# Kernel optimization log

Measured on AMD Instinct MI355X. Metric: run time of the kernel, lower is better.

## Reference

```python
import jax, jax.numpy as jnp
import numpy as np

INPUT_SIZE = 1024
HIDDEN_SIZE = 1024
BATCH = 8192


def setup_inputs() -> dict:
    key = jax.random.key(0)
    ks = jax.random.split(key, 10)
    H, I, B = HIDDEN_SIZE, INPUT_SIZE, BATCH
    s = 1.0 / np.sqrt(H)  # scale params so activations stay in sane range
    return {
        "input": jax.random.normal(ks[0], (B, I), jnp.float32),
        "hx": jax.random.normal(ks[1], (B, H), jnp.float32),
        "cx": jax.random.normal(ks[2], (B, H), jnp.float32),
        "att": jax.random.normal(ks[3], (B, I), jnp.float32),
        "weight_ih": jax.random.normal(ks[4], (4 * H, I), jnp.float32) * s,
        "weight_hh": jax.random.normal(ks[5], (4 * H, H), jnp.float32) * s,
        "bias_ih": jax.random.normal(ks[6], (4 * H,), jnp.float32),
        "bias_hh": jax.random.normal(ks[7], (4 * H,), jnp.float32),
        "weight_att": jax.random.normal(ks[8], (2 * H, I), jnp.float32) * s,
        "bias_att": jax.random.normal(ks[9], (2 * H,), jnp.float32),
    }


def reference(input, hx, cx, att, weight_ih, weight_hh, bias_ih, bias_hh,
              weight_att, bias_att):
    H = weight_hh.shape[1]
    # gates: [B, 4H]
    gates = input @ weight_ih.T + bias_ih + hx @ weight_hh.T + bias_hh
    att_gates = att @ weight_att.T + bias_att  # [B, 2H]
    ingate, forgetgate, cellgate, outgate = jnp.split(gates, 4, axis=1)
    ingate_att, attgate = jnp.split(att_gates, 2, axis=1)
    ingate = jax.nn.sigmoid(ingate)
    forgetgate = jax.nn.sigmoid(forgetgate)
    cellgate = jnp.tanh(cellgate)
    ingate_att = jax.nn.sigmoid(ingate_att)
    attgate = jnp.tanh(attgate)
    outgate = jax.nn.sigmoid(outgate)
    cy = forgetgate * cx + ingate * cellgate + ingate_att * attgate
    hy = outgate * jnp.tanh(cy)
    return (hy, cy)
```

## Files before the change

kernel.cpp:

```cpp
#include <hip/hip_runtime.h>


typedef __attribute__((ext_vector_type(8))) __bf16 bf16x8;
typedef __attribute__((ext_vector_type(8))) unsigned short ushort8;
typedef __attribute__((ext_vector_type(4))) float f32x4;

#define AS1 __attribute__((address_space(1)))
#define AS3 __attribute__((address_space(3)))

__device__ __forceinline__ void gld16(const unsigned short* g, unsigned short* l) {
    __builtin_amdgcn_global_load_lds((const AS1 void*)g, (AS3 void*)l, 16, 0, 0);
}

__device__ __forceinline__ unsigned short f2bf(float f) {
    unsigned int u = __builtin_bit_cast(unsigned int, f);
    u += 0x7fffu + ((u >> 16) & 1u);
    return (unsigned short)(u >> 16);
}

__device__ __forceinline__ float sigmoidf_(float x) { return 1.f / (1.f + __expf(-x)); }
__device__ __forceinline__ float tanhf_(float x) {
    float e = __expf(-2.f * fabsf(x));
    float t = (1.f - e) / (1.f + e);
    return x >= 0.f ? t : -t;
}

__device__ __forceinline__ bf16x8 ldfrag(const unsigned short* p) {
    return __builtin_bit_cast(bf16x8, *(const ushort8*)p);
}

#define BARRIER __builtin_amdgcn_s_barrier()
#define LGKM0   asm volatile("s_waitcnt lgkmcnt(0)" ::: "memory")
#define VMW_(n) asm volatile("s_waitcnt vmcnt(" #n ")" ::: "memory")
#define VMW(n)  VMW_(n)
#define MFMA16(a, b, c) __builtin_amdgcn_mfma_f32_16x16x32_bf16(a, b, c, 0, 0, 0)

__global__ void cast_all_k(const float* __restrict__ input, const float* __restrict__ hx,
                           const float* __restrict__ att,   const float* __restrict__ w_ih,
                           const float* __restrict__ w_hh,  const float* __restrict__ w_att,
                           const float* __restrict__ b_ih,  const float* __restrict__ b_hh,
                           unsigned short* __restrict__ XH, unsigned short* __restrict__ ATTb,
                           unsigned short* __restrict__ W4, unsigned short* __restrict__ WA,
                           float* __restrict__ bias4)
{
    int gid = blockIdx.x * blockDim.x + threadIdx.x;
    if (gid < 4096) bias4[gid] = b_ih[gid] + b_hh[gid];
    const int total = 4456448;
    for (int i = gid; i < total; i += gridDim.x * blockDim.x) {
        const float* src; unsigned short* dst; int ld, off, rel;
        if (i < 1048576)      { src = input; dst = XH;   ld = 2048; off = 0;    rel = i; }
        else if (i < 2097152) { src = hx;    dst = XH;   ld = 2048; off = 1024; rel = i - 1048576; }
        else if (i < 3145728) { src = att;   dst = ATTb; ld = 1024; off = 0;    rel = i - 2097152; }
        else if (i < 3670016) { src = w_ih;  dst = W4;   ld = 2048; off = 0;    rel = i - 3145728; }
        else if (i < 4194304) { src = w_hh;  dst = W4;   ld = 2048; off = 1024; rel = i - 3670016; }
        else                  { src = w_att; dst = WA;   ld = 1024; off = 0;    rel = i - 4194304; }
        int e = rel * 8;
        int r = e >> 10, c = e & 1023;
        const float4 v0 = *(const float4*)(src + e);
        const float4 v1 = *(const float4*)(src + e + 4);
        ushort8 p;
        p[0] = f2bf(v0.x); p[1] = f2bf(v0.y); p[2] = f2bf(v0.z); p[3] = f2bf(v0.w);
        p[4] = f2bf(v1.x); p[5] = f2bf(v1.y); p[6] = f2bf(v1.z); p[7] = f2bf(v1.w);
        *(ushort8*)(dst + r * ld + off + c) = p;
    }
}

__global__ __launch_bounds__(512, 2) void fused_gemm_k(
    const unsigned short* __restrict__ XH, const unsigned short* __restrict__ W4,
    const unsigned short* __restrict__ ATTb, const unsigned short* __restrict__ WA,
    const float* __restrict__ bias4, const float* __restrict__ bias_att,
    const float* __restrict__ cx, float* __restrict__ out)
{
    __shared__ unsigned short As[2][16384];
    __shared__ unsigned short Bs[2][16384];

    const int tid  = threadIdx.x;
    const int wave = tid >> 6, lane = tid & 63;
    const int l15 = lane & 15, quad = lane >> 4;
    const int wr = wave >> 2, wn = wave & 3;

    const int orig = blockIdx.x;
    const int wg   = (orig & 7) * 64 + (orig >> 3);
    const int row0 = (wg & 31) * 256;
    const int n0   = (wg >> 5) * 64;

    const int rl = tid >> 3;
    const int c8 = (tid & 7) ^ (rl & 7);
    unsigned aG = (unsigned)(row0 + rl) * 2048u + (unsigned)c8 * 8u;
    unsigned bG = (unsigned)(((rl >> 4) & 3) * 1024 + n0 + (rl & 15)) * 2048u + (unsigned)c8 * 8u;
    unsigned aA = (unsigned)(row0 + rl) * 1024u + (unsigned)c8 * 8u;
    unsigned bA = (unsigned)(((rl >> 4) & 1) * 1024 + n0 + ((rl >> 5) & 1) * 16 + (rl & 15)) * 1024u
                  + (unsigned)c8 * 8u;

    auto stageA_att = [&](int buf) {
#pragma unroll
        for (int h = 0; h < 2; ++h)
#pragma unroll
            for (int p = 0; p < 2; ++p)
                gld16(ATTb + aA + (unsigned)(h * 131072 + p * 65536),
                      &As[buf][h * 8192 + (tid + p * 512) * 8]);
        aA += 64;
    };
    auto stageB_att = [&](int buf) {
#pragma unroll
        for (int h = 0; h < 2; ++h)
            gld16(WA + bA + (unsigned)(h * 32768), &Bs[buf][(h * 512 + tid) * 8]);
        bA += 64;
    };
    auto stageA_g = [&](int buf) {
#pragma unroll
        for (int h = 0; h < 2; ++h)
#pragma unroll
            for (int p = 0; p < 2; ++p)
                gld16(XH + aG + (unsigned)(h * 262144 + p * 131072),
                      &As[buf][h * 8192 + (tid + p * 512) * 8]);
        aG += 64;
    };
    auto stageB_g = [&](int buf) {
#pragma unroll
        for (int h = 0; h < 2; ++h)
#pragma unroll
            for (int p = 0; p < 2; ++p)
                gld16(W4 + bG + (unsigned)(h * 65536 + p * 32768),
                      &Bs[buf][h * 8192 + (tid + p * 512) * 8]);
        bG += 64;
    };

    const int swz0 = (quad ^ (l15 & 7)) * 8;
    const int swz1 = ((4 + quad) ^ (l15 & 7)) * 8;
    const int aro  = (wr * 128 + l15) * 64;
    const int brG  = (wn * 64 + l15) * 64;
    const int brA  = (wn * 32 + l15) * 64;

    const f32x4 z = {0.f, 0.f, 0.f, 0.f};

    f32x4 acc2[8][2];
#pragma unroll
    for (int i = 0; i < 8; ++i) { acc2[i][0] = z; acc2[i][1] = z; }

    auto att_group = [&](int buf, bool issA, bool issB) {
        bf16x8 aF[4][2], bLo[2][2];
#pragma unroll
        for (int i = 0; i < 4; ++i) {
            aF[i][0] = ldfrag(&As[buf][aro + i * 1024 + swz0]);
            aF[i][1] = ldfrag(&As[buf][aro + i * 1024 + swz1]);
        }
#pragma unroll
        for (int j = 0; j < 2; ++j) {
            bLo[j][0] = ldfrag(&Bs[buf][brA + j * 1024 + swz0]);
            bLo[j][1] = ldfrag(&Bs[buf][brA + j * 1024 + swz1]);
        }
        if (issA) stageA_att(buf ^ 1);
        BARRIER; LGKM0;
        __builtin_amdgcn_s_setprio(1);
#pragma unroll
        for (int i = 0; i < 4; ++i)
#pragma unroll
            for (int j = 0; j < 2; ++j) {
                acc2[i][j] = MFMA16(aF[i][0], bLo[j][0], acc2[i][j]);
                acc2[i][j] = MFMA16(aF[i][1], bLo[j][1], acc2[i][j]);
            }
        __builtin_amdgcn_s_setprio(0);
        BARRIER;
#pragma unroll
        for (int i = 0; i < 4; ++i) {
            aF[i][0] = ldfrag(&As[buf][aro + (4 + i) * 1024 + swz0]);
            aF[i][1] = ldfrag(&As[buf][aro + (4 + i) * 1024 + swz1]);
        }
        if (issB) stageB_att(buf);
        BARRIER; LGKM0;
        __builtin_amdgcn_s_setprio(1);
#pragma unroll
        for (int i = 0; i < 4; ++i)
#pragma unroll
            for (int j = 0; j < 2; ++j) {
                acc2[4 + i][j] = MFMA16(aF[i][0], bLo[j][0], acc2[4 + i][j]);
                acc2[4 + i][j] = MFMA16(aF[i][1], bLo[j][1], acc2[4 + i][j]);
            }
        __builtin_amdgcn_s_setprio(0);
    };

    stageA_att(0); stageB_att(0); stageB_att(1);
    VMW(2); BARRIER;
#pragma unroll 2
    for (int t = 0; t < 14; ++t) {
        att_group(t & 1, true, true);
        VMW(2); BARRIER;
    }
    att_group(0, true, false);  VMW(0); BARRIER;
    att_group(1, false, false); BARRIER;

    const int col = n0 + wn * 16 + l15;
    f32x4 attp[8];
    {
        const float ba0 = bias_att[col], ba1 = bias_att[1024 + col];
#pragma unroll
        for (int i = 0; i < 8; ++i)
#pragma unroll
            for (int r = 0; r < 4; ++r)
                attp[i][r] = sigmoidf_(acc2[i][0][r] + ba0) * tanhf_(acc2[i][1][r] + ba1);
    }

    f32x4 acc[8][4];
#pragma unroll
    for (int i = 0; i < 8; ++i)
#pragma unroll
        for (int j = 0; j < 4; ++j) acc[i][j] = z;

    auto gates_group = [&](int buf, bool iss) {
        bf16x8 aF[4][2], bLo[2][2], bHi[2][2];
#pragma unroll
        for (int i = 0; i < 4; ++i) {
            aF[i][0] = ldfrag(&As[buf][aro + i * 1024 + swz0]);
            aF[i][1] = ldfrag(&As[buf][aro + i * 1024 + swz1]);
        }
#pragma unroll
        for (int j = 0; j < 2; ++j) {
            bLo[j][0] = ldfrag(&Bs[buf][brG + j * 1024 + swz0]);
            bLo[j][1] = ldfrag(&Bs[buf][brG + j * 1024 + swz1]);
        }
        BARRIER; LGKM0;
        __builtin_amdgcn_s_setprio(1);
#pragma unroll
        for (int i = 0; i < 4; ++i)
#pragma unroll
            for (int j = 0; j < 2; ++j) {
                acc[i][j] = MFMA16(aF[i][0], bLo[j][0], acc[i][j]);
                acc[i][j] = MFMA16(aF[i][1], bLo[j][1], acc[i][j]);
            }
        __builtin_amdgcn_s_setprio(0);
        BARRIER;
#pragma unroll
        for (int j = 0; j < 2; ++j) {
            bHi[j][0] = ldfrag(&Bs[buf][brG + (2 + j) * 1024 + swz0]);
            bHi[j][1] = ldfrag(&Bs[buf][brG + (2 + j) * 1024 + swz1]);
        }
        BARRIER; LGKM0;
        __builtin_amdgcn_s_setprio(1);
#pragma unroll
        for (int i = 0; i < 4; ++i)
#pragma unroll
            for (int j = 0; j < 2; ++j) {
                acc[i][2 + j] = MFMA16(aF[i][0], bHi[j][0], acc[i][2 + j]);
                acc[i][2 + j] = MFMA16(aF[i][1], bHi[j][1], acc[i][2 + j]);
            }
        __builtin_amdgcn_s_setprio(0);
        BARRIER;
#pragma unroll
        for (int i = 0; i < 4; ++i) {
            aF[i][0] = ldfrag(&As[buf][aro + (4 + i) * 1024 + swz0]);
            aF[i][1] = ldfrag(&As[buf][aro + (4 + i) * 1024 + swz1]);
        }
        if (iss) stageB_g(buf);
        BARRIER; LGKM0;
        __builtin_amdgcn_s_setprio(1);
#pragma unroll
        for (int i = 0; i < 4; ++i)
#pragma unroll
            for (int j = 0; j < 2; ++j) {
                acc[4 + i][2 + j] = MFMA16(aF[i][0], bHi[j][0], acc[4 + i][2 + j]);
                acc[4 + i][2 + j] = MFMA16(aF[i][1], bHi[j][1], acc[4 + i][2 + j]);
            }
        __builtin_amdgcn_s_setprio(0);
        BARRIER;
        if (iss) stageA_g(buf);
        BARRIER;
        __builtin_amdgcn_s_setprio(1);
#pragma unroll
        for (int i = 0; i < 4; ++i)
#pragma unroll
            for (int j = 0; j < 2; ++j) {
                acc[4 + i][j] = MFMA16(aF[i][0], bLo[j][0], acc[4 + i][j]);
                acc[4 + i][j] = MFMA16(aF[i][1], bLo[j][1], acc[4 + i][j]);
            }
        __builtin_amdgcn_s_setprio(0);
    };

    stageA_g(0); stageB_g(0); stageA_g(1); stageB_g(1);
    VMW(8); BARRIER;
#pragma unroll 2
    for (int t = 0; t < 30; ++t) {
        gates_group(t & 1, true);
        VMW(8); BARRIER;
    }
    gates_group(0, false); VMW(0); BARRIER;
    gates_group(1, false);

    const int Rb = row0 + wr * 128 + quad * 4;
    const float bi  = bias4[col];
    const float bff = bias4[1024 + col];
    const float bg  = bias4[2048 + col];
    const float bo  = bias4[3072 + col];
    const int CYOFF = 8192 * 1024;
#pragma unroll
    for (int i = 0; i < 8; ++i) {
#pragma unroll
        for (int r = 0; r < 4; ++r) {
            const int R   = Rb + i * 16 + r;
            const int off = R * 1024 + col;
            float ig = sigmoidf_(acc[i][0][r] + bi);
            float fg = sigmoidf_(acc[i][1][r] + bff);
            float gg = tanhf_(acc[i][2][r] + bg);
            float og = sigmoidf_(acc[i][3][r] + bo);
            float cyv = fg * cx[off] + ig * gg + attp[i][r];
            float hyv = og * tanhf_(cyv);
            out[off] = hyv;
            out[CYOFF + off] = cyv;
        }
    }
}

extern "C" void kernel_launch(void* const* d_in, const int* in_sizes, int n_in,
                              void* d_out, int out_size, void* d_ws, size_t ws_size,
                              hipStream_t stream) {
    const float* input = (const float*)d_in[0];
    const float* hx    = (const float*)d_in[1];
    const float* cx    = (const float*)d_in[2];
    const float* att   = (const float*)d_in[3];
    const float* w_ih  = (const float*)d_in[4];
    const float* w_hh  = (const float*)d_in[5];
    const float* b_ih  = (const float*)d_in[6];
    const float* b_hh  = (const float*)d_in[7];
    const float* w_att = (const float*)d_in[8];
    const float* b_att = (const float*)d_in[9];
    float* out = (float*)d_out;

    char* ws = (char*)d_ws;
    unsigned short* XH   = (unsigned short*)(ws);
    unsigned short* ATTb = (unsigned short*)(ws + 33554432);
    unsigned short* W4   = (unsigned short*)(ws + 50331648);
    unsigned short* WA   = (unsigned short*)(ws + 67108864);
    float* bias4         = (float*)(ws + 71303168);

    cast_all_k<<<8704, 256, 0, stream>>>(input, hx, att, w_ih, w_hh, w_att,
                                         b_ih, b_hh, XH, ATTb, W4, WA, bias4);
    fused_gemm_k<<<512, 512, 0, stream>>>(XH, W4, ATTb, WA, bias4, b_att, cx, out);
}
```

Measured before the change: 422.9 us.

## Restructure GEMM pipelines, remap XCD tiles, and stage epilogue through LDS

```diff
diff --git a/kernel.cpp b/kernel.cpp
--- a/kernel.cpp
+++ b/kernel.cpp
@@ -33,6 +33,8 @@
 #define LGKM0   asm volatile("s_waitcnt lgkmcnt(0)" ::: "memory")
 #define VMW_(n) asm volatile("s_waitcnt vmcnt(" #n ")" ::: "memory")
 #define VMW(n)  VMW_(n)
+#define PRIO1   __builtin_amdgcn_s_setprio(1)
+#define PRIO0   __builtin_amdgcn_s_setprio(0)
 #define MFMA16(a, b, c) __builtin_amdgcn_mfma_f32_16x16x32_bf16(a, b, c, 0, 0, 0)
 
 __global__ void cast_all_k(const float* __restrict__ input, const float* __restrict__ hx,
@@ -80,9 +82,9 @@
     const int wr = wave >> 2, wn = wave & 3;
 
     const int orig = blockIdx.x;
-    const int wg   = (orig & 7) * 64 + (orig >> 3);
-    const int row0 = (wg & 31) * 256;
-    const int n0   = (wg >> 5) * 64;
+    const int k    = orig >> 3, xcd = orig & 7;
+    const int row0 = (k >> 1) * 256;
+    const int n0   = (xcd * 2 + (k & 1)) * 64;
 
     const int rl = tid >> 3;
     const int c8 = (tid & 7) ^ (rl & 7);
@@ -138,57 +140,35 @@
 #pragma unroll
     for (int i = 0; i < 8; ++i) { acc2[i][0] = z; acc2[i][1] = z; }
 
-    auto att_group = [&](int buf, bool issA, bool issB) {
-        bf16x8 aF[4][2], bLo[2][2];
-#pragma unroll
-        for (int i = 0; i < 4; ++i) {
-            aF[i][0] = ldfrag(&As[buf][aro + i * 1024 + swz0]);
-            aF[i][1] = ldfrag(&As[buf][aro + i * 1024 + swz1]);
-        }
-#pragma unroll
-        for (int j = 0; j < 2; ++j) {
-            bLo[j][0] = ldfrag(&Bs[buf][brA + j * 1024 + swz0]);
-            bLo[j][1] = ldfrag(&Bs[buf][brA + j * 1024 + swz1]);
-        }
-        if (issA) stageA_att(buf ^ 1);
+    auto att_slice = [&](int buf, int sw) {
+        bf16x8 aS[8], bS[2];
+#pragma unroll
+        for (int i = 0; i < 8; ++i) aS[i] = ldfrag(&As[buf][aro + i * 1024 + sw]);
+#pragma unroll
+        for (int j = 0; j < 2; ++j) bS[j] = ldfrag(&Bs[buf][brA + j * 1024 + sw]);
         BARRIER; LGKM0;
-        __builtin_amdgcn_s_setprio(1);
-#pragma unroll
-        for (int i = 0; i < 4; ++i)
-#pragma unroll
-            for (int j = 0; j < 2; ++j) {
-                acc2[i][j] = MFMA16(aF[i][0], bLo[j][0], acc2[i][j]);
-                acc2[i][j] = MFMA16(aF[i][1], bLo[j][1], acc2[i][j]);
-            }
-        __builtin_amdgcn_s_setprio(0);
-        BARRIER;
-#pragma unroll
-        for (int i = 0; i < 4; ++i) {
-            aF[i][0] = ldfrag(&As[buf][aro + (4 + i) * 1024 + swz0]);
-            aF[i][1] = ldfrag(&As[buf][aro + (4 + i) * 1024 + swz1]);
-        }
-        if (issB) stageB_att(buf);
-        BARRIER; LGKM0;
-        __builtin_amdgcn_s_setprio(1);
-#pragma unroll
-        for (int i = 0; i < 4; ++i)
-#pragma unroll
-            for (int j = 0; j < 2; ++j) {
-                acc2[4 + i][j] = MFMA16(aF[i][0], bLo[j][0], acc2[4 + i][j]);
-                acc2[4 + i][j] = MFMA16(aF[i][1], bLo[j][1], acc2[4 + i][j]);
-            }
-        __builtin_amdgcn_s_setprio(0);
-    };
-
-    stageA_att(0); stageB_att(0); stageB_att(1);
-    VMW(2); BARRIER;
-#pragma unroll 2
-    for (int t = 0; t < 14; ++t) {
-        att_group(t & 1, true, true);
-        VMW(2); BARRIER;
-    }
-    att_group(0, true, false);  VMW(0); BARRIER;
-    att_group(1, false, false); BARRIER;
+        PRIO1;
+#pragma unroll
+        for (int i = 0; i < 8; ++i)
+#pragma unroll
+            for (int j = 0; j < 2; ++j)
+                acc2[i][j] = MFMA16(aS[i], bS[j], acc2[i][j]);
+        PRIO0;
+        BARRIER;
+    };
+
+    stageA_att(0); stageB_att(0);
+    for (int g = 0; g < 8; ++g) {
+        stageA_att(1); stageB_att(1);
+        VMW(6); BARRIER;
+        att_slice(0, swz0);
+        att_slice(0, swz1);
+        if (g < 7) { stageA_att(0); stageB_att(0); VMW(6); }
+        else       { VMW(0); }
+        BARRIER;
+        att_slice(1, swz0);
+        att_slice(1, swz1);
+    }
 
     const int col = n0 + wn * 16 + l15;
     f32x4 attp[8];
@@ -208,72 +188,56 @@
         for (int j = 0; j < 4; ++j) acc[i][j] = z;
 
     auto gates_group = [&](int buf, bool iss) {
-        bf16x8 aF[4][2], bLo[2][2], bHi[2][2];
+        bf16x8 aF[4], aH0[4], aH1[4], bS0[4], bS1[4];
+#pragma unroll
+        for (int i = 0; i < 4; ++i) aF[i] = ldfrag(&As[buf][aro + i * 1024 + swz0]);
+#pragma unroll
+        for (int j = 0; j < 4; ++j) bS0[j] = ldfrag(&Bs[buf][brG + j * 1024 + swz0]);
+        BARRIER; LGKM0;
+        PRIO1;
+#pragma unroll
+        for (int i = 0; i < 4; ++i)
+#pragma unroll
+            for (int j = 0; j < 4; ++j)
+                acc[i][j] = MFMA16(aF[i], bS0[j], acc[i][j]);
+        PRIO0;
+        BARRIER;
+#pragma unroll
+        for (int i = 0; i < 4; ++i) aF[i] = ldfrag(&As[buf][aro + i * 1024 + swz1]);
+#pragma unroll
+        for (int j = 0; j < 4; ++j) bS1[j] = ldfrag(&Bs[buf][brG + j * 1024 + swz1]);
+        BARRIER; LGKM0;
+        PRIO1;
+#pragma unroll
+        for (int i = 0; i < 4; ++i)
+#pragma unroll
+            for (int j = 0; j < 4; ++j)
+                acc[i][j] = MFMA16(aF[i], bS1[j], acc[i][j]);
+        PRIO0;
+        BARRIER;
 #pragma unroll
         for (int i = 0; i < 4; ++i) {
-            aF[i][0] = ldfrag(&As[buf][aro + i * 1024 + swz0]);
-            aF[i][1] = ldfrag(&As[buf][aro + i * 1024 + swz1]);
-        }
-#pragma unroll
-        for (int j = 0; j < 2; ++j) {
-            bLo[j][0] = ldfrag(&Bs[buf][brG + j * 1024 + swz0]);
-            bLo[j][1] = ldfrag(&Bs[buf][brG + j * 1024 + swz1]);
-        }
-        BARRIER; LGKM0;
-        __builtin_amdgcn_s_setprio(1);
-#pragma unroll
-        for (int i = 0; i < 4; ++i)
-#pragma unroll
-            for (int j = 0; j < 2; ++j) {
-                acc[i][j] = MFMA16(aF[i][0], bLo[j][0], acc[i][j]);
-                acc[i][j] = MFMA16(aF[i][1], bLo[j][1], acc[i][j]);
-            }
-        __builtin_amdgcn_s_setprio(0);
-        BARRIER;
-#pragma unroll
-        for (int j = 0; j < 2; ++j) {
-            bHi[j][0] = ldfrag(&Bs[buf][brG + (2 + j) * 1024 + swz0]);
-            bHi[j][1] = ldfrag(&Bs[buf][brG + (2 + j) * 1024 + swz1]);
-        }
-        BARRIER; LGKM0;
-        __builtin_amdgcn_s_setprio(1);
-#pragma unroll
-        for (int i = 0; i < 4; ++i)
-#pragma unroll
-            for (int j = 0; j < 2; ++j) {
-                acc[i][2 + j] = MFMA16(aF[i][0], bHi[j][0], acc[i][2 + j]);
-                acc[i][2 + j] = MFMA16(aF[i][1], bHi[j][1], acc[i][2 + j]);
-            }
-        __builtin_amdgcn_s_setprio(0);
-        BARRIER;
-#pragma unroll
-        for (int i = 0; i < 4; ++i) {
-            aF[i][0] = ldfrag(&As[buf][aro + (4 + i) * 1024 + swz0]);
-            aF[i][1] = ldfrag(&As[buf][aro + (4 + i) * 1024 + swz1]);
+            aH0[i] = ldfrag(&As[buf][aro + (4 + i) * 1024 + swz0]);
+            aH1[i] = ldfrag(&As[buf][aro + (4 + i) * 1024 + swz1]);
         }
         if (iss) stageB_g(buf);
         BARRIER; LGKM0;
-        __builtin_amdgcn_s_setprio(1);
+        PRIO1;
 #pragma unroll
         for (int i = 0; i < 4; ++i)
 #pragma unroll
-            for (int j = 0; j < 2; ++j) {
-                acc[4 + i][2 + j] = MFMA16(aF[i][0], bHi[j][0], acc[4 + i][2 + j]);
-                acc[4 + i][2 + j] = MFMA16(aF[i][1], bHi[j][1], acc[4 + i][2 + j]);
-            }
-        __builtin_amdgcn_s_setprio(0);
+            for (int j = 0; j < 4; ++j)
+                acc[4 + i][j] = MFMA16(aH0[i], bS0[j], acc[4 + i][j]);
+        PRIO0;
         BARRIER;
         if (iss) stageA_g(buf);
-        BARRIER;
-        __builtin_amdgcn_s_setprio(1);
+        PRIO1;
 #pragma unroll
         for (int i = 0; i < 4; ++i)
 #pragma unroll
-            for (int j = 0; j < 2; ++j) {
-                acc[4 + i][j] = MFMA16(aF[i][0], bLo[j][0], acc[4 + i][j]);
-                acc[4 + i][j] = MFMA16(aF[i][1], bLo[j][1], acc[4 + i][j]);
-            }
-        __builtin_amdgcn_s_setprio(0);
+            for (int j = 0; j < 4; ++j)
+                acc[4 + i][j] = MFMA16(aH1[i], bS1[j], acc[4 + i][j]);
+        PRIO0;
     };
 
     stageA_g(0); stageB_g(0); stageA_g(1); stageB_g(1);
@@ -286,27 +250,68 @@
     gates_group(0, false); VMW(0); BARRIER;
     gates_group(1, false);
 
-    const int Rb = row0 + wr * 128 + quad * 4;
+    float* sF = (float*)(&As[0][0]);
+    float* sC = (float*)(&Bs[0][0]);
     const float bi  = bias4[col];
     const float bff = bias4[1024 + col];
     const float bg  = bias4[2048 + col];
     const float bo  = bias4[3072 + col];
+    const int lcol  = wn * 16 + l15;
     const int CYOFF = 8192 * 1024;
-#pragma unroll
-    for (int i = 0; i < 8; ++i) {
+
+#pragma unroll
+    for (int i = 0; i < 8; ++i)
 #pragma unroll
         for (int r = 0; r < 4; ++r) {
-            const int R   = Rb + i * 16 + r;
-            const int off = R * 1024 + col;
-            float ig = sigmoidf_(acc[i][0][r] + bi);
-            float fg = sigmoidf_(acc[i][1][r] + bff);
-            float gg = tanhf_(acc[i][2][r] + bg);
-            float og = sigmoidf_(acc[i][3][r] + bo);
-            float cyv = fg * cx[off] + ig * gg + attp[i][r];
-            float hyv = og * tanhf_(cyv);
-            out[off] = hyv;
-            out[CYOFF + off] = cyv;
+            const int lr = wr * 128 + i * 16 + quad * 4 + r;
+            const int pc = lcol ^ (((lr >> 2) & 1) << 4);
+            sF[lr * 64 + pc] = sigmoidf_(acc[i][1][r] + bff);
+            sC[lr * 64 + pc] = sigmoidf_(acc[i][0][r] + bi) * tanhf_(acc[i][2][r] + bg)
+                               + attp[i][r];
         }
+    BARRIER;
+
+    const int rr = tid >> 4;
+    const int cc = (tid & 15) * 4;
+#pragma unroll
+    for (int p = 0; p < 8; ++p) {
+        const int row = p * 32 + rr;
+        const int pcc = cc ^ (((row >> 2) & 1) << 4);
+        f32x4 fg4 = *(f32x4*)&sF[row * 64 + pcc];
+        f32x4 cp4 = *(f32x4*)&sC[row * 64 + pcc];
+        const float4 cx4 = *(const float4*)&cx[(row0 + row) * 1024 + n0 + cc];
+        f32x4 cy4;
+        cy4[0] = fg4[0] * cx4.x + cp4[0];
+        cy4[1] = fg4[1] * cx4.y + cp4[1];
+        cy4[2] = fg4[2] * cx4.z + cp4[2];
+        cy4[3] = fg4[3] * cx4.w + cp4[3];
+        *(f32x4*)&out[CYOFF + (row0 + row) * 1024 + n0 + cc] = cy4;
+        *(f32x4*)&sF[row * 64 + pcc] = cy4;
+    }
+    BARRIER;
+
+#pragma unroll
+    for (int i = 0; i < 8; ++i)
+#pragma unroll
+        for (int r = 0; r < 4; ++r) {
+            const int lr = wr * 128 + i * 16 + quad * 4 + r;
+            const int pc = lcol ^ (((lr >> 2) & 1) << 4);
+            sC[lr * 64 + pc] = sigmoidf_(acc[i][3][r] + bo);
+        }
+    BARRIER;
+
+#pragma unroll
+    for (int p = 0; p < 8; ++p) {
+        const int row = p * 32 + rr;
+        const int pcc = cc ^ (((row >> 2) & 1) << 4);
+        f32x4 og4 = *(f32x4*)&sC[row * 64 + pcc];
+        f32x4 cy4 = *(f32x4*)&sF[row * 64 + pcc];
+        f32x4 hy4;
+        hy4[0] = og4[0] * tanhf_(cy4[0]);
+        hy4[1] = og4[1] * tanhf_(cy4[1]);
+        hy4[2] = og4[2] * tanhf_(cy4[2]);
+        hy4[3] = og4[3] * tanhf_(cy4[3]);
+        *(f32x4*)&out[(row0 + row) * 1024 + n0 + cc] = hy4;
     }
 }
 
```

Result: faster. 403.4 us (-4.6%).
